# Kernel optimization log

Hardware: AMD Instinct MI355X
Metric: run time of the kernel (lower is better)

## Reference

```python
import jax, jax.numpy as jnp
import numpy as np

B = 4096        # batch_size (world_size = 1)
D = 128         # embedding dim
TEMP = 0.5      # temperature
EPS = 1e-8      # torch CosineSimilarity eps
BIG = 1e9       # diagonal masking constant


def setup_inputs() -> dict:
    key = jax.random.key(0)
    k1, k2 = jax.random.split(key)
    z_i = jax.random.normal(k1, (B, D), dtype=jnp.float32)
    z_j = jax.random.normal(k2, (B, D), dtype=jnp.float32)
    return {"z_i": z_i, "z_j": z_j}


def reference(z_i, z_j):
    N = 2 * B
    z = jnp.concatenate([z_i, z_j], axis=0)                    # [N, D]
    # cosine similarity: normalize once, then a single GEMM (avoids NxNxD)
    norm = jnp.maximum(jnp.linalg.norm(z, axis=1, keepdims=True), EPS)
    zn = z / norm                                              # [N, D]
    sim = (zn @ zn.T) / TEMP                                   # [N, N]
    # mask self-similarity on the diagonal
    sim = sim - BIG * jnp.eye(N, dtype=sim.dtype)
    # positive of row i is i+B (first half) or i-B (second half)
    labels = jnp.concatenate([jnp.arange(B) + B, jnp.arange(B)])  # [N]
    # cross-entropy, reduction='sum', then divide by N
    logp = jax.nn.log_softmax(sim, axis=1)                     # [N, N]
    loss = -jnp.sum(jnp.take_along_axis(logp, labels[:, None], axis=1)) / N
    return loss
```

## Files before the change

### kernel.cpp

```cpp
#include <hip/hip_runtime.h>
#include <hip/hip_bf16.h>
#include <hip/hip_fp16.h>

#define NB   4096
#define NTOT 8192
#define DD   128
#define ROWB 256
#define NSLOT 64

typedef __attribute__((ext_vector_type(8))) _Float16 f16x8;
typedef __attribute__((ext_vector_type(4))) float    f32x4;

#if defined(__has_builtin)
#if __has_builtin(__builtin_amdgcn_exp2f)
#define EXP2F(x) __builtin_amdgcn_exp2f(x)
#else
#define EXP2F(x) exp2f(x)
#endif
#if __has_builtin(__builtin_amdgcn_logf)
#define LOG2F(x) __builtin_amdgcn_logf(x)
#else
#define LOG2F(x) log2f(x)
#endif
#else
#define EXP2F(x) exp2f(x)
#define LOG2F(x) log2f(x)
#endif

#define SQSCALE 1.69864394f
#define LN2     0.69314718056f


__global__ void knorm(const float* __restrict__ zi, const float* __restrict__ zj,
                      _Float16* __restrict__ zs, float* __restrict__ out) {
  int wave = threadIdx.x >> 6, lane = threadIdx.x & 63;
  int j = lane & 31;
  int row = (blockIdx.x << 3) + (wave << 1) + (lane >> 5);
  const float* src = (row < NB) ? (zi + (size_t)row * DD)
                                : (zj + (size_t)(row - NB) * DD);
  float4 v = ((const float4*)src)[j];
  float ss = v.x * v.x + v.y * v.y + v.z * v.z + v.w * v.w;
#pragma unroll
  for (int m = 1; m < 32; m <<= 1) ss += __shfl_xor(ss, m, 64);
  float inv = SQSCALE / fmaxf(sqrtf(ss), 1e-8f);
  struct H4 { _Float16 a, b, c, d; } hv;
  hv.a = (_Float16)(v.x * inv); hv.b = (_Float16)(v.y * inv);
  hv.c = (_Float16)(v.z * inv); hv.d = (_Float16)(v.w * inv);
  int phys = (j >> 1) ^ (row & 15);
  char* dst = (char*)zs + (size_t)row * ROWB + phys * 16 + (j & 1) * 8;
  *(uint2*)dst = __builtin_bit_cast(uint2, hv);
  if (blockIdx.x == 0 && threadIdx.x == 0) out[0] = 0.f;
}

__device__ __forceinline__ void gl_lds16(const char* g, char* l) {
  __builtin_amdgcn_global_load_lds(
      (const __attribute__((address_space(1))) void*)g,
      (__attribute__((address_space(3))) void*)l, 16, 0, 0);
}

__global__ __launch_bounds__(256) void kmain(const _Float16* __restrict__ zs,
                                             float* __restrict__ partial,
                                             float* __restrict__ slabel) {
  int rb = blockIdx.x >> 6;
  int cb = blockIdx.x & 63;
  if (cb < rb) return;
  __shared__ f16x8 sB[2][1024];
  int wave  = threadIdx.x >> 6;
  int lane  = threadIdx.x & 63;
  int q = lane >> 4;
  int c = lane & 15;
  int d = c - (q << 2);
  int rowbase = rb * 128 + wave * 32;
  int colchunk = cb * 128;
  bool diagblk = (rb == cb);

  f16x8 a[2][4];
#pragma unroll
  for (int st = 0; st < 2; st++) {
    const char* p = (const char*)zs + (size_t)(rowbase + st * 16 + c) * ROWB;
#pragma unroll
    for (int kk = 0; kk < 4; kk++)
      a[st][kk] = *(const f16x8*)(p + (((kk << 2) + q) ^ c) * 16);
  }

  float part[2][4] = {{0.f,0.f,0.f,0.f},{0.f,0.f,0.f,0.f}};
  float cpart[8] = {0,0,0,0,0,0,0,0};

  const char* gB = (const char*)zs + (size_t)colchunk * ROWB;
  int soff = wave * 4096 + lane * 16;

  auto stage = [&](int s) {
    const char* g = gB + (size_t)s * (64 * ROWB) + soff;
    char* l = (char*)&sB[s & 1][0] + soff;
    gl_lds16(g, l);
    gl_lds16(g + 1024, l + 1024);
    gl_lds16(g + 2048, l + 2048);
    gl_lds16(g + 3072, l + 3072);
  };

  auto compute = [&](int s) {
    const char* base = (const char*)&sB[s & 1][0];
#pragma unroll
    for (int t = 0; t < 4; t++) {
      int tt = s * 4 + t;
      int colbase = colchunk + tt * 16;
      f16x8 b[4];
      const char* bp = base + (t * 16 + c) * ROWB;
#pragma unroll
      for (int kk = 0; kk < 4; kk++)
        b[kk] = *(const f16x8*)(bp + (((kk << 2) + q) ^ c) * 16);
#pragma unroll
      for (int st = 0; st < 2; st++) {
        int sbase = rowbase + st * 16;
        f32x4 acc = {0.f, 0.f, 0.f, 0.f};
#pragma unroll
        for (int kk = 0; kk < 4; kk++)
          acc = __builtin_amdgcn_mfma_f32_16x16x32_f16(a[st][kk], b[kk], acc, 0, 0, 0);
        if (colbase == (sbase ^ NB)) {
#pragma unroll
          for (int r = 0; r < 4; r++)
            if (d == r) {
              slabel[sbase + c] = acc[r];
              slabel[(sbase + c) ^ NB] = acc[r];
            }
        }
        if (colbase == sbase) {
#pragma unroll
          for (int r = 0; r < 4; r++) {
            float e = (d == r) ? 0.f : EXP2F(acc[r]);
            part[st][r] += e;
            cpart[tt]   += e;
          }
        } else {
#pragma unroll
          for (int r = 0; r < 4; r++) {
            float e = EXP2F(acc[r]);
            part[st][r] += e;
            cpart[tt]   += e;
          }
        }
      }
    }
  };

  stage(0);
  __syncthreads();
  for (int s = 0; s < 2; s++) {
    if (s + 1 < 2) stage(s + 1);
    compute(s);
    __syncthreads();
  }

  float* ebuf  = (float*)&sB[0][0];
  float* cwave = ebuf + 128;

#pragma unroll
  for (int st = 0; st < 2; st++)
#pragma unroll
    for (int r = 0; r < 4; r++) {
      float v = part[st][r];
      v += __shfl_xor(v, 1, 64);
      v += __shfl_xor(v, 2, 64);
      v += __shfl_xor(v, 4, 64);
      v += __shfl_xor(v, 8, 64);
      if (c == 0) ebuf[wave * 32 + st * 16 + (q << 2) + r] = v;
    }
  if (!diagblk) {
#pragma unroll
    for (int tt = 0; tt < 8; tt++) {
      float v = cpart[tt];
      v += __shfl_xor(v, 16, 64);
      v += __shfl_xor(v, 32, 64);
      if (q == 0) cwave[wave * 128 + tt * 16 + c] = v;
    }
  }
  __syncthreads();
  if (threadIdx.x < 128) {
    partial[(size_t)cb * NTOT + rb * 128 + threadIdx.x] = ebuf[threadIdx.x];
  } else if (!diagblk) {
    int col = threadIdx.x - 128;
    float s = cwave[col] + cwave[128 + col] + cwave[256 + col] + cwave[384 + col];
    partial[(size_t)rb * NTOT + cb * 128 + col] = s;
  }
}

__global__ void kfinal(const float* __restrict__ partial,
                       const float* __restrict__ slabel,
                       float* __restrict__ out) {
  int i = blockIdx.x * 256 + threadIdx.x;
  float s = 0.f;
#pragma unroll 8
  for (int k = 0; k < NSLOT; k++) s += partial[(size_t)k * NTOT + i];
  float acc = LN2 * (LOG2F(s) - slabel[i]);
#pragma unroll
  for (int m = 1; m < 64; m <<= 1) acc += __shfl_xor(acc, m, 64);
  __shared__ float wsum[4];
  int tid = threadIdx.x;
  if ((tid & 63) == 0) wsum[tid >> 6] = acc;
  __syncthreads();
  if (tid == 0)
    atomicAdd(out, (wsum[0] + wsum[1] + wsum[2] + wsum[3]) * (1.0f / (float)NTOT));
}

extern "C" void kernel_launch(void* const* d_in, const int* in_sizes, int n_in,
                              void* d_out, int out_size, void* d_ws, size_t ws_size,
                              hipStream_t stream) {
  const float* zi = (const float*)d_in[0];
  const float* zj = (const float*)d_in[1];
  float* out = (float*)d_out;

  char* ws = (char*)d_ws;
  const size_t ZS_BYTES = (size_t)NTOT * DD * sizeof(_Float16);
  _Float16* zs   = (_Float16*)ws;
  float* partial = (float*)(ws + ZS_BYTES);
  float* slabel  = (float*)(ws + ZS_BYTES + (size_t)NSLOT * NTOT * 4);

  knorm<<<NTOT / 8, 256, 0, stream>>>(zi, zj, zs, out);
  kmain<<<64 * 64, 256, 0, stream>>>(zs, partial, slabel);
  kfinal<<<NTOT / 256, 256, 0, stream>>>(partial, slabel, out);
}
```

Baseline: 89.10 us.

## Make main kernel persistent over upper-triangle tiles with balanced static partition

Replaces the 64x64 grid, where lower-triangle blocks exit immediately, with 512 persistent blocks. Each block walks a contiguous range of the 2080 upper-triangular tiles, finding its starting tile by inverting the triangular index. The next column tile is double-buffered into shared memory while the current one is computed, and A fragments are reloaded only when the row block changes. This removes launch and early-exit overhead for idle blocks and overlaps tile loads with compute. In exchange, shared memory per block doubles and each tile ends with a full barrier.

```diff
diff --git a/kernel.cpp b/kernel.cpp
--- a/kernel.cpp
+++ b/kernel.cpp
@@ -1,6 +1,7 @@
 #include <hip/hip_runtime.h>
 #include <hip/hip_bf16.h>
 #include <hip/hip_fp16.h>
+#include <math.h>
 
 #define NB   4096
 #define NTOT 8192
@@ -61,51 +62,61 @@
 __global__ __launch_bounds__(256) void kmain(const _Float16* __restrict__ zs,
                                              float* __restrict__ partial,
                                              float* __restrict__ slabel) {
-  int rb = blockIdx.x >> 6;
-  int cb = blockIdx.x & 63;
-  if (cb < rb) return;
-  __shared__ f16x8 sB[2][1024];
-  int wave  = threadIdx.x >> 6;
-  int lane  = threadIdx.x & 63;
+  __shared__ f16x8 sB[2][2048];
+  __shared__ float cw[2][4][128];
+  int p  = blockIdx.x;
+  int t0 = (p * 65) >> 4;
+  int t1 = ((p + 1) * 65) >> 4;
+  int n  = t1 - t0;
+  int wave = threadIdx.x >> 6, lane = threadIdx.x & 63;
   int q = lane >> 4;
   int c = lane & 15;
   int d = c - (q << 2);
-  int rowbase = rb * 128 + wave * 32;
-  int colchunk = cb * 128;
-  bool diagblk = (rb == cb);
+
+  int rb = (int)(64.5 - sqrt(64.5 * 64.5 - 2.0 * (double)t0));
+  while (64 * (rb + 1) - ((rb + 1) * rb) / 2 <= t0) rb++;
+  while (64 * rb - (rb * (rb - 1)) / 2 > t0) rb--;
+  int cb = rb + (t0 - (64 * rb - (rb * (rb - 1)) / 2));
 
   f16x8 a[2][4];
-#pragma unroll
-  for (int st = 0; st < 2; st++) {
-    const char* p = (const char*)zs + (size_t)(rowbase + st * 16 + c) * ROWB;
-#pragma unroll
-    for (int kk = 0; kk < 4; kk++)
-      a[st][kk] = *(const f16x8*)(p + (((kk << 2) + q) ^ c) * 16);
-  }
-
-  float part[2][4] = {{0.f,0.f,0.f,0.f},{0.f,0.f,0.f,0.f}};
-  float cpart[8] = {0,0,0,0,0,0,0,0};
-
-  const char* gB = (const char*)zs + (size_t)colchunk * ROWB;
-  int soff = wave * 4096 + lane * 16;
-
-  auto stage = [&](int s) {
-    const char* g = gB + (size_t)s * (64 * ROWB) + soff;
-    char* l = (char*)&sB[s & 1][0] + soff;
-    gl_lds16(g, l);
-    gl_lds16(g + 1024, l + 1024);
-    gl_lds16(g + 2048, l + 2048);
-    gl_lds16(g + 3072, l + 3072);
+  auto loadA = [&](int r) {
+#pragma unroll
+    for (int st = 0; st < 2; st++) {
+      const char* pp = (const char*)zs +
+                       (size_t)(r * 128 + wave * 32 + st * 16 + c) * ROWB;
+#pragma unroll
+      for (int kk = 0; kk < 4; kk++)
+        a[st][kk] = *(const f16x8*)(pp + (((kk << 2) + q) ^ c) * 16);
+    }
   };
-
-  auto compute = [&](int s) {
-    const char* base = (const char*)&sB[s & 1][0];
-#pragma unroll
-    for (int t = 0; t < 4; t++) {
-      int tt = s * 4 + t;
+  auto stage = [&](int col_b, int par) {
+    const char* g = (const char*)zs + (size_t)col_b * 128 * ROWB + threadIdx.x * 16;
+    char* l = (char*)&sB[par][0] + threadIdx.x * 16;
+#pragma unroll
+    for (int i = 0; i < 8; i++) gl_lds16(g + i * 4096, l + i * 4096);
+  };
+
+  loadA(rb);
+  stage(cb, 0);
+  __syncthreads();
+  int par = 0;
+
+  for (int i = 0; i < n; i++) {
+    int nrb = rb, ncb = cb + 1;
+    if (ncb == 64) { nrb = rb + 1; ncb = nrb; }
+    if (i + 1 < n) stage(ncb, par ^ 1);
+
+    int rowbase = rb * 128 + wave * 32;
+    int colchunk = cb * 128;
+    bool diag = (rb == cb);
+    float part[2][4] = {{0.f,0.f,0.f,0.f},{0.f,0.f,0.f,0.f}};
+    float cpart[8] = {0,0,0,0,0,0,0,0};
+
+#pragma unroll
+    for (int tt = 0; tt < 8; tt++) {
       int colbase = colchunk + tt * 16;
       f16x8 b[4];
-      const char* bp = base + (t * 16 + c) * ROWB;
+      const char* bp = (const char*)&sB[par][0] + (tt * 16 + c) * ROWB;
 #pragma unroll
       for (int kk = 0; kk < 4; kk++)
         b[kk] = *(const f16x8*)(bp + (((kk << 2) + q) ^ c) * 16);
@@ -128,59 +139,48 @@
 #pragma unroll
           for (int r = 0; r < 4; r++) {
             float e = (d == r) ? 0.f : EXP2F(acc[r]);
-            part[st][r] += e;
-            cpart[tt]   += e;
+            part[st][r] += e; cpart[tt] += e;
           }
         } else {
 #pragma unroll
           for (int r = 0; r < 4; r++) {
             float e = EXP2F(acc[r]);
-            part[st][r] += e;
-            cpart[tt]   += e;
+            part[st][r] += e; cpart[tt] += e;
           }
         }
       }
     }
-  };
-
-  stage(0);
-  __syncthreads();
-  for (int s = 0; s < 2; s++) {
-    if (s + 1 < 2) stage(s + 1);
-    compute(s);
+
+#pragma unroll
+    for (int st = 0; st < 2; st++)
+#pragma unroll
+      for (int r = 0; r < 4; r++) {
+        float v = part[st][r];
+        v += __shfl_xor(v, 1, 64);
+        v += __shfl_xor(v, 2, 64);
+        v += __shfl_xor(v, 4, 64);
+        v += __shfl_xor(v, 8, 64);
+        if (c == 0)
+          partial[(size_t)cb * NTOT + rowbase + st * 16 + (q << 2) + r] = v;
+      }
+    if (!diag) {
+#pragma unroll
+      for (int tt = 0; tt < 8; tt++) {
+        float v = cpart[tt];
+        v += __shfl_xor(v, 16, 64);
+        v += __shfl_xor(v, 32, 64);
+        if (q == 0) cw[par][wave][tt * 16 + c] = v;
+      }
+    }
     __syncthreads();
-  }
-
-  float* ebuf  = (float*)&sB[0][0];
-  float* cwave = ebuf + 128;
-
-#pragma unroll
-  for (int st = 0; st < 2; st++)
-#pragma unroll
-    for (int r = 0; r < 4; r++) {
-      float v = part[st][r];
-      v += __shfl_xor(v, 1, 64);
-      v += __shfl_xor(v, 2, 64);
-      v += __shfl_xor(v, 4, 64);
-      v += __shfl_xor(v, 8, 64);
-      if (c == 0) ebuf[wave * 32 + st * 16 + (q << 2) + r] = v;
-    }
-  if (!diagblk) {
-#pragma unroll
-    for (int tt = 0; tt < 8; tt++) {
-      float v = cpart[tt];
-      v += __shfl_xor(v, 16, 64);
-      v += __shfl_xor(v, 32, 64);
-      if (q == 0) cwave[wave * 128 + tt * 16 + c] = v;
-    }
-  }
-  __syncthreads();
-  if (threadIdx.x < 128) {
-    partial[(size_t)cb * NTOT + rb * 128 + threadIdx.x] = ebuf[threadIdx.x];
-  } else if (!diagblk) {
-    int col = threadIdx.x - 128;
-    float s = cwave[col] + cwave[128 + col] + cwave[256 + col] + cwave[384 + col];
-    partial[(size_t)rb * NTOT + cb * 128 + col] = s;
+    if (!diag && threadIdx.x < 128) {
+      int col = threadIdx.x;
+      float s = cw[par][0][col] + cw[par][1][col] +
+                cw[par][2][col] + cw[par][3][col];
+      partial[(size_t)rb * NTOT + colchunk + col] = s;
+    }
+    if (i + 1 < n && nrb != rb) loadA(nrb);
+    rb = nrb; cb = ncb; par ^= 1;
   }
 }
 
@@ -216,6 +216,6 @@
   float* slabel  = (float*)(ws + ZS_BYTES + (size_t)NSLOT * NTOT * 4);
 
   knorm<<<NTOT / 8, 256, 0, stream>>>(zi, zj, zs, out);
-  kmain<<<64 * 64, 256, 0, stream>>>(zs, partial, slabel);
+  kmain<<<512, 256, 0, stream>>>(zs, partial, slabel);
   kfinal<<<NTOT / 256, 256, 0, stream>>>(partial, slabel, out);
 }
```

Measured after the change: 90.15 us. About the same (+1.2%).
